# Kernel optimization log

Measured on AMD Instinct MI355X. Metric: run time of the kernel, lower is better.

## Reference

```python
import jax, jax.numpy as jnp
import numpy as np

B, S, N, F = 32, 50, 2000, 3
D = 64
E = 1_000_000
NUM_NODES = B * N


def setup_inputs() -> dict:
    key = jax.random.key(0)
    ks = jax.random.split(key, 8)
    x = jax.random.normal(ks[0], (B, S, N, F), dtype=jnp.float32)
    edge_index = jax.random.randint(ks[1], (2, E), 0, NUM_NODES, dtype=jnp.int64)
    # Glorot-ish init for parameters
    W1 = jax.random.normal(ks[2], (F, D), dtype=jnp.float32) * (1.0 / np.sqrt(F))
    b1 = jnp.zeros((D,), dtype=jnp.float32)
    W2 = jax.random.normal(ks[3], (D, D), dtype=jnp.float32) * (1.0 / np.sqrt(D))
    b2 = jnp.zeros((D,), dtype=jnp.float32)
    Wh = jax.random.normal(ks[4], (D, 2), dtype=jnp.float32) * (1.0 / np.sqrt(D))
    bh = jnp.zeros((2,), dtype=jnp.float32)
    return {"x": x, "edge_index": edge_index, "W1": W1, "b1": b1,
            "W2": W2, "b2": b2, "Wh": Wh, "bh": bh}


def reference(x, edge_index, W1, b1, W2, b2, Wh, bh):
    b, s, n, f = x.shape
    num_nodes = b * n
    h0 = x.mean(axis=1).reshape(num_nodes, f)  # temporal mean, flatten batch graphs

    # GCN normalization with self-loops (PyG GCNConv defaults)
    loops = jnp.arange(num_nodes, dtype=edge_index.dtype)
    src = jnp.concatenate([edge_index[0], loops])
    dst = jnp.concatenate([edge_index[1], loops])
    deg = jax.ops.segment_sum(jnp.ones_like(src, dtype=h0.dtype), dst,
                              num_segments=num_nodes)
    dinv = jnp.where(deg > 0, jax.lax.rsqrt(deg), 0.0)
    norm = dinv[src] * dinv[dst]  # per-edge weight

    def gcn(h, W, bias):
        h = h @ W                                  # transform first (out <= in)
        msg = h[src] * norm[:, None]               # gather + scale
        agg = jax.ops.segment_sum(msg, dst, num_segments=num_nodes)  # scatter-add
        return agg + bias

    h = jax.nn.relu(gcn(h0, W1, b1))
    h = jax.nn.relu(gcn(h, W2, b2))
    # global_mean_pool with batch = arange(B).repeat_interleave(N) == per-graph mean
    pooled = h.reshape(b, n, -1).mean(axis=1)
    return pooled @ Wh + bh
```

## Files before the change

### kernel.cpp

```cpp
#include <hip/hip_runtime.h>
#include <hip/hip_bf16.h>
#include <hip/hip_fp16.h>
#include <cstdint>

#define NV 64000
#define DD 64
#define FF 3
#define NE 1000000
#define BB 32
#define SS 50
#define NN 2000
#define KB 1000
#define CAP 1536
#define NBLKA 250
#define EPB (NE / NBLKA)
#define TMB 750
#define INVALID 0xFFFFFFFFu
#define RPW 16
#define NWAVES (NV / RPW)
#define WPG (NN / RPW)
#define RST 20

__global__ __launch_bounds__(256) void setup_kernel(const int* __restrict__ ei,
                                                    int* __restrict__ flag,
                                                    int* __restrict__ gcur) {
    int i = blockIdx.x * 256 + threadIdx.x;
    if (i < KB) gcur[i] = 0;
    if (blockIdx.x == 0) {
        __shared__ int nz;
        if (threadIdx.x == 0) nz = 0;
        __syncthreads();
        int local = 0;
        for (int k = threadIdx.x; k < 4096; k += 256)
            local |= (ei[2 * k + 1] != 0);
        if (local) atomicOr(&nz, 1);
        __syncthreads();
        if (threadIdx.x == 0) *flag = (nz == 0) ? 1 : 0;
    }
}

__global__ __launch_bounds__(256) void part_tmean_kernel(const int* __restrict__ ei32,
                                                         const int* __restrict__ flag,
                                                         int* __restrict__ gcur,
                                                         unsigned* __restrict__ parts,
                                                         const float* __restrict__ x,
                                                         float* __restrict__ p0) {
    __shared__ unsigned recs[EPB];
    __shared__ int cnt[KB];
    __shared__ int cur[KB];
    int t = threadIdx.x;
    if (blockIdx.x >= NBLKA) {
        int tid = (blockIdx.x - NBLKA) * 256 + t;
        int nf = tid % (NN * FF);
        int b  = tid / (NN * FF);
        const float* xp = x + (size_t)b * SS * NN * FF + nf;
        float acc = 0.f;
        #pragma unroll
        for (int s = 0; s < SS; ++s) acc += xp[(size_t)s * NN * FF];
        p0[tid] = acc * (1.0f / SS);
        return;
    }
    const long long* ei64 = (const long long*)ei32;
    const int is64 = *flag;
    int e0 = blockIdx.x * EPB;
    for (int i = t; i < KB; i += 256) cnt[i] = 0;
    __syncthreads();
    for (int i = t; i < EPB; i += 256) {
        int e = e0 + i;
        int s, d;
        if (is64) { s = (int)ei64[e]; d = (int)ei64[NE + e]; }
        else      { s = ei32[e];      d = ei32[NE + e]; }
        bool ok = (unsigned)s < NV && (unsigned)d < NV;
        recs[i] = ok ? (((unsigned)s << 16) | (unsigned)d) : INVALID;
        if (ok) atomicAdd(&cnt[d >> 6], 1);
    }
    __syncthreads();
    for (int b = t; b < KB; b += 256) {
        int c = cnt[b];
        cur[b] = (c > 0) ? atomicAdd(&gcur[b], c) : 0;
    }
    __syncthreads();
    for (int i = t; i < EPB; i += 256) {
        unsigned r = recs[i];
        if (r != INVALID) {
            int d = (int)(r & 0xFFFFu);
            int b = d >> 6;
            int pos = atomicAdd(&cur[b], 1);
            if (pos < CAP)
                parts[(size_t)b * CAP + pos] = ((r >> 16) << 6) | (unsigned)(d & 63);
        }
    }
}

__global__ __launch_bounds__(256) void bsort_kernel(unsigned* __restrict__ parts,
                                                    const int* __restrict__ gcur,
                                                    int* __restrict__ beg,
                                                    int* __restrict__ end,
                                                    float* __restrict__ dinv,
                                                    float* __restrict__ p0) {
    __shared__ unsigned recs[CAP];
    __shared__ int srt[CAP];
    __shared__ int cnt64[64];
    __shared__ int pref[64];
    __shared__ int cur[64];
    int b = blockIdx.x, t = threadIdx.x;
    int cnt = min(gcur[b], CAP);
    unsigned* p = parts + (size_t)b * CAP;
    if (t < 64) cnt64[t] = 0;
    __syncthreads();
    for (int i = t; i < cnt; i += 256) {
        unsigned r = p[i];
        recs[i] = r;
        atomicAdd(&cnt64[r & 63u], 1);
    }
    __syncthreads();
    if (t < 64) pref[t] = cnt64[t];
    __syncthreads();
    #pragma unroll
    for (int off = 1; off < 64; off <<= 1) {
        int v = (t < 64 && t >= off) ? pref[t - off] : 0;
        __syncthreads();
        if (t < 64) pref[t] += v;
        __syncthreads();
    }
    if (t < 64) {
        int ex = pref[t] - cnt64[t];
        cur[t] = ex;
        int node = (b << 6) + t;
        beg[node] = b * CAP + ex;
        end[node] = b * CAP + ex + cnt64[t];
        dinv[node] = rsqrtf((float)(cnt64[t] + 1));
    }
    __syncthreads();
    for (int i = t; i < cnt; i += 256) {
        unsigned r = recs[i];
        int pos = atomicAdd(&cur[r & 63u], 1);
        srt[pos] = (int)(r >> 6);
    }
    __syncthreads();
    for (int i = t; i < cnt; i += 256) p[i] = (unsigned)srt[i];
    for (int i = t; i < 64 * FF; i += 256) {
        float dv = rsqrtf((float)(cnt64[i / FF] + 1));
        p0[(size_t)b * 64 * FF + i] *= dv;
    }
}

__global__ __launch_bounds__(256) void agg3_kernel(const int* __restrict__ beg,
                                                   const int* __restrict__ end,
                                                   const unsigned* __restrict__ srcs,
                                                   const float* __restrict__ p0,
                                                   const float* __restrict__ dinv,
                                                   float4* __restrict__ q04) {
    int node = blockIdx.x * 256 + threadIdx.x;
    if (node >= NV) return;
    int e = beg[node], en = end[node];
    float a0 = p0[node * 3 + 0], a1 = p0[node * 3 + 1], a2 = p0[node * 3 + 2];
    for (; e + 2 <= en; e += 2) {
        int s0 = srcs[e] * 3, s1 = srcs[e + 1] * 3;
        float u0 = p0[s0], u1 = p0[s0 + 1], u2 = p0[s0 + 2];
        float w0 = p0[s1], w1 = p0[s1 + 1], w2 = p0[s1 + 2];
        a0 += u0 + w0; a1 += u1 + w1; a2 += u2 + w2;
    }
    for (; e < en; ++e) {
        int s = srcs[e] * 3;
        a0 += p0[s]; a1 += p0[s + 1]; a2 += p0[s + 2];
    }
    q04[node] = make_float4(a0, a1, a2, dinv[node]);
}

__global__ void trans1_kernel(const float4* __restrict__ q04,
                              const float* __restrict__ W1, const float* __restrict__ b1,
                              __half2* __restrict__ p1h) {
    int tid = blockIdx.x * blockDim.x + threadIdx.x;
    if (tid >= NV * 32) return;
    int node = tid >> 5, j = tid & 31;
    int d0 = 2 * j, d1 = 2 * j + 1;
    float4 q = q04[node];
    float h0 = fmaf(q.w, fmaf(q.x, W1[d0], fmaf(q.y, W1[64 + d0], q.z * W1[128 + d0])), b1[d0]);
    float h1 = fmaf(q.w, fmaf(q.x, W1[d1], fmaf(q.y, W1[64 + d1], q.z * W1[128 + d1])), b1[d1]);
    p1h[tid] = __floats2half2_rn(q.w * fmaxf(h0, 0.f), q.w * fmaxf(h1, 0.f));
}

__global__ __launch_bounds__(256) void agg64_kernel(const int* __restrict__ beg,
                                                    const int* __restrict__ end,
                                                    const unsigned* __restrict__ srcs,
                                                    const __half2* __restrict__ g,
                                                    float* __restrict__ raw) {
    int lane = threadIdx.x & 63;
    int node = (blockIdx.x * blockDim.x + threadIdx.x) >> 6;
    if (node >= NV) return;
    int grp = lane >> 3, sub = lane & 7;
    const uint4* base = (const uint4*)g;
    float a0 = 0.f, a1 = 0.f, a2 = 0.f, a3 = 0.f;
    float a4 = 0.f, a5 = 0.f, a6 = 0.f, a7 = 0.f;
#define UNPACK_ADD(v) do { float2 f_;                                         \
        f_ = __half22float2(*(const __half2*)&(v).x); a0 += f_.x; a1 += f_.y; \
        f_ = __half22float2(*(const __half2*)&(v).y); a2 += f_.x; a3 += f_.y; \
        f_ = __half22float2(*(const __half2*)&(v).z); a4 += f_.x; a5 += f_.y; \
        f_ = __half22float2(*(const __half2*)&(v).w); a6 += f_.x; a7 += f_.y; } while (0)
    if (grp == 0) {
        uint4 v = base[((size_t)node << 3) + sub];
        UNPACK_ADD(v);
    }
    int e = beg[node] + grp, en = end[node];
    for (; e + 8 < en; e += 16) {
        uint4 v0 = base[((size_t)srcs[e] << 3) + sub];
        uint4 v1 = base[((size_t)srcs[e + 8] << 3) + sub];
        UNPACK_ADD(v0);
        UNPACK_ADD(v1);
    }
    if (e < en) {
        uint4 v = base[((size_t)srcs[e] << 3) + sub];
        UNPACK_ADD(v);
    }
#undef UNPACK_ADD
    #pragma unroll
    for (int m = 8; m <= 32; m <<= 1) {
        a0 += __shfl_xor(a0, m); a1 += __shfl_xor(a1, m);
        a2 += __shfl_xor(a2, m); a3 += __shfl_xor(a3, m);
        a4 += __shfl_xor(a4, m); a5 += __shfl_xor(a5, m);
        a6 += __shfl_xor(a6, m); a7 += __shfl_xor(a7, m);
    }
    if (grp == 0) {
        float4* out = (float4*)(raw + ((size_t)node << 6));
        out[sub * 2 + 0] = make_float4(a0, a1, a2, a3);
        out[sub * 2 + 1] = make_float4(a4, a5, a6, a7);
    }
}

__global__ __launch_bounds__(256) void trans2pool_kernel(const float* __restrict__ q1,
                                                         const float* __restrict__ dinv,
                                                         const float* __restrict__ b2,
                                                         const float* __restrict__ W2,
                                                         float* __restrict__ partials) {
    __shared__ float w2s[64 * 64];
    __shared__ float rT[4][64 * RST];
    int t = threadIdx.x;
    int lane = t & 63, wvid = t >> 6;
    for (int i = t; i < 64 * 64; i += 256) w2s[i] = W2[i];

    int wid = blockIdx.x * 4 + wvid;
    int n0 = wid * RPW;
    float v[16];
    #pragma unroll
    for (int i = 0; i < 16; ++i) v[i] = q1[((size_t)(n0 + i) << 6) + lane];
    float* rw = rT[wvid];
    #pragma unroll
    for (int r0 = 0; r0 < 16; r0 += 4)
        *(float4*)&rw[lane * RST + r0] = make_float4(v[r0], v[r0 + 1], v[r0 + 2], v[r0 + 3]);
    __syncthreads();

    int ri0 = (lane >> 4) * 4;
    int c0 = (lane & 15) * 4;
    float acc00 = 0.f, acc01 = 0.f, acc02 = 0.f, acc03 = 0.f;
    float acc10 = 0.f, acc11 = 0.f, acc12 = 0.f, acc13 = 0.f;
    float acc20 = 0.f, acc21 = 0.f, acc22 = 0.f, acc23 = 0.f;
    float acc30 = 0.f, acc31 = 0.f, acc32 = 0.f, acc33 = 0.f;
    #pragma unroll 2
    for (int k = 0; k < 64; ++k) {
        float4 w4 = *(const float4*)&w2s[k * 64 + c0];
        float4 r4 = *(const float4*)&rw[k * RST + ri0];
        acc00 = fmaf(r4.x, w4.x, acc00); acc01 = fmaf(r4.x, w4.y, acc01);
        acc02 = fmaf(r4.x, w4.z, acc02); acc03 = fmaf(r4.x, w4.w, acc03);
        acc10 = fmaf(r4.y, w4.x, acc10); acc11 = fmaf(r4.y, w4.y, acc11);
        acc12 = fmaf(r4.y, w4.z, acc12); acc13 = fmaf(r4.y, w4.w, acc13);
        acc20 = fmaf(r4.z, w4.x, acc20); acc21 = fmaf(r4.z, w4.y, acc21);
        acc22 = fmaf(r4.z, w4.z, acc22); acc23 = fmaf(r4.z, w4.w, acc23);
        acc30 = fmaf(r4.w, w4.x, acc30); acc31 = fmaf(r4.w, w4.y, acc31);
        acc32 = fmaf(r4.w, w4.z, acc32); acc33 = fmaf(r4.w, w4.w, acc33);
    }
    float4 bv = *(const float4*)&b2[c0];
    float d0 = dinv[n0 + ri0 + 0], d1 = dinv[n0 + ri0 + 1];
    float d2 = dinv[n0 + ri0 + 2], d3 = dinv[n0 + ri0 + 3];
    float s0 = fmaxf(fmaf(d0, acc00, bv.x), 0.f) + fmaxf(fmaf(d1, acc10, bv.x), 0.f)
             + fmaxf(fmaf(d2, acc20, bv.x), 0.f) + fmaxf(fmaf(d3, acc30, bv.x), 0.f);
    float s1 = fmaxf(fmaf(d0, acc01, bv.y), 0.f) + fmaxf(fmaf(d1, acc11, bv.y), 0.f)
             + fmaxf(fmaf(d2, acc21, bv.y), 0.f) + fmaxf(fmaf(d3, acc31, bv.y), 0.f);
    float s2 = fmaxf(fmaf(d0, acc02, bv.z), 0.f) + fmaxf(fmaf(d1, acc12, bv.z), 0.f)
             + fmaxf(fmaf(d2, acc22, bv.z), 0.f) + fmaxf(fmaf(d3, acc32, bv.z), 0.f);
    float s3 = fmaxf(fmaf(d0, acc03, bv.w), 0.f) + fmaxf(fmaf(d1, acc13, bv.w), 0.f)
             + fmaxf(fmaf(d2, acc23, bv.w), 0.f) + fmaxf(fmaf(d3, acc33, bv.w), 0.f);
    s0 += __shfl_xor(s0, 16); s1 += __shfl_xor(s1, 16);
    s2 += __shfl_xor(s2, 16); s3 += __shfl_xor(s3, 16);
    s0 += __shfl_xor(s0, 32); s1 += __shfl_xor(s1, 32);
    s2 += __shfl_xor(s2, 32); s3 += __shfl_xor(s3, 32);
    if (lane < 16)
        *(float4*)&partials[(size_t)wid * 64 + c0] = make_float4(s0, s1, s2, s3);
}

__global__ __launch_bounds__(256) void pool_finish_kernel(const float* __restrict__ partials,
                                                          const float* __restrict__ Wh,
                                                          const float* __restrict__ bh,
                                                          float* __restrict__ out) {
    __shared__ float part[4][64];
    __shared__ float pooled[64];
    int b = blockIdx.x;
    int t = threadIdx.x;
    int d = t & 63, g = t >> 6;
    float s = 0.f;
    for (int c = g; c < WPG; c += 4)
        s += partials[((size_t)(b * WPG + c)) * 64 + d];
    part[g][d] = s;
    __syncthreads();
    if (t < 64)
        pooled[t] = (part[0][t] + part[1][t] + part[2][t] + part[3][t]) * (1.0f / NN);
    __syncthreads();
    if (t < 2) {
        float o = bh[t];
        #pragma unroll 16
        for (int k = 0; k < 64; ++k) o += pooled[k] * Wh[k * 2 + t];
        out[b * 2 + t] = o;
    }
}

extern "C" void kernel_launch(void* const* d_in, const int* in_sizes, int n_in,
                              void* d_out, int out_size, void* d_ws, size_t ws_size,
                              hipStream_t stream) {
    const float* x  = (const float*)d_in[0];
    const int*   ei = (const int*)d_in[1];
    const float* W1 = (const float*)d_in[2];
    const float* b1 = (const float*)d_in[3];
    const float* W2 = (const float*)d_in[4];
    const float* b2 = (const float*)d_in[5];
    const float* Wh = (const float*)d_in[6];
    const float* bh = (const float*)d_in[7];
    float* out = (float*)d_out;

    float* ws   = (float*)d_ws;
    float* bufA = ws;
    float* bufB = bufA + (size_t)NV * DD;
    float* p0   = bufB + (size_t)NV * DD;
    float4* q04 = (float4*)(p0 + (size_t)NV * FF);
    float* dinv = (float*)(q04 + NV);
    float* partials = dinv + NV;
    unsigned* parts = (unsigned*)(partials + (size_t)NWAVES * 64);
    int*   beg  = (int*)(parts + (size_t)KB * CAP);
    int*   end  = beg + NV;
    int*   gcur = end + NV;
    int*   flag = gcur + KB;
    __half2* p1h = (__half2*)bufA;

    setup_kernel<<<4, 256, 0, stream>>>(ei, flag, gcur);
    part_tmean_kernel<<<NBLKA + TMB, 256, 0, stream>>>(ei, flag, gcur, parts, x, p0);

    bsort_kernel<<<KB, 256, 0, stream>>>(parts, gcur, beg, end, dinv, p0);

    agg3_kernel<<<(NV + 255) / 256, 256, 0, stream>>>(beg, end, parts, p0, dinv, q04);

    trans1_kernel<<<NV * 32 / 256, 256, 0, stream>>>(q04, W1, b1, p1h);

    agg64_kernel<<<NV * 64 / 256, 256, 0, stream>>>(beg, end, parts, p1h, bufB);

    trans2pool_kernel<<<NWAVES / 4, 256, 0, stream>>>(bufB, dinv, b2, W2, partials);

    pool_finish_kernel<<<BB, 256, 0, stream>>>(partials, Wh, bh, out);
}
```

Before: 105.4 us.

## Fuse dtype detection into partition kernel, merge agg3 with trans1, store agg64 in half

Removes the setup kernel by having each partition block detect the int64 edge format itself and clearing the bucket counters with a memset. The 3-wide aggregation is fused with the first linear transform through a shared-memory staging of per-node float4s, which eliminates the q04 round trip and one launch. The 64-wide aggregation output is now written as fp16 instead of fp32, halving its write and the following read in trans2pool. In exchange, every partition block redundantly scans 4096 index words, and the layer-2 pre-activations lose some precision.

Measured after the change: 101.1 us, median of 2. -4.1%, faster.

```diff
diff --git a/kernel.cpp b/kernel.cpp
--- a/kernel.cpp
+++ b/kernel.cpp
@@ -21,33 +21,11 @@
 #define WPG (NN / RPW)
 #define RST 20
 
-__global__ __launch_bounds__(256) void setup_kernel(const int* __restrict__ ei,
-                                                    int* __restrict__ flag,
-                                                    int* __restrict__ gcur) {
-    int i = blockIdx.x * 256 + threadIdx.x;
-    if (i < KB) gcur[i] = 0;
-    if (blockIdx.x == 0) {
-        __shared__ int nz;
-        if (threadIdx.x == 0) nz = 0;
-        __syncthreads();
-        int local = 0;
-        for (int k = threadIdx.x; k < 4096; k += 256)
-            local |= (ei[2 * k + 1] != 0);
-        if (local) atomicOr(&nz, 1);
-        __syncthreads();
-        if (threadIdx.x == 0) *flag = (nz == 0) ? 1 : 0;
-    }
-}
-
 __global__ __launch_bounds__(256) void part_tmean_kernel(const int* __restrict__ ei32,
-                                                         const int* __restrict__ flag,
                                                          int* __restrict__ gcur,
                                                          unsigned* __restrict__ parts,
                                                          const float* __restrict__ x,
                                                          float* __restrict__ p0) {
-    __shared__ unsigned recs[EPB];
-    __shared__ int cnt[KB];
-    __shared__ int cur[KB];
     int t = threadIdx.x;
     if (blockIdx.x >= NBLKA) {
         int tid = (blockIdx.x - NBLKA) * 256 + t;
@@ -60,11 +38,20 @@
         p0[tid] = acc * (1.0f / SS);
         return;
     }
+    __shared__ unsigned recs[EPB];
+    __shared__ int cnt[KB];
+    __shared__ int cur[KB];
+    __shared__ int nz;
+    if (t == 0) nz = 0;
+    for (int i = t; i < KB; i += 256) cnt[i] = 0;
+    __syncthreads();
+    int local = 0;
+    for (int k = t; k < 4096; k += 256) local |= (ei32[2 * k + 1] != 0);
+    if (local) atomicOr(&nz, 1);
+    __syncthreads();
+    const int is64 = (nz == 0);
     const long long* ei64 = (const long long*)ei32;
-    const int is64 = *flag;
     int e0 = blockIdx.x * EPB;
-    for (int i = t; i < KB; i += 256) cnt[i] = 0;
-    __syncthreads();
     for (int i = t; i < EPB; i += 256) {
         int e = e0 + i;
         int s, d;
@@ -145,14 +132,17 @@
     }
 }
 
-__global__ __launch_bounds__(256) void agg3_kernel(const int* __restrict__ beg,
-                                                   const int* __restrict__ end,
-                                                   const unsigned* __restrict__ srcs,
-                                                   const float* __restrict__ p0,
-                                                   const float* __restrict__ dinv,
-                                                   float4* __restrict__ q04) {
-    int node = blockIdx.x * 256 + threadIdx.x;
-    if (node >= NV) return;
+__global__ __launch_bounds__(256) void agg3trans_kernel(const int* __restrict__ beg,
+                                                        const int* __restrict__ end,
+                                                        const unsigned* __restrict__ srcs,
+                                                        const float* __restrict__ p0,
+                                                        const float* __restrict__ dinv,
+                                                        const float* __restrict__ W1,
+                                                        const float* __restrict__ b1,
+                                                        __half2* __restrict__ p1h) {
+    __shared__ float4 q4s[256];
+    int t = threadIdx.x;
+    int node = blockIdx.x * 256 + t;
     int e = beg[node], en = end[node];
     float a0 = p0[node * 3 + 0], a1 = p0[node * 3 + 1], a2 = p0[node * 3 + 2];
     for (; e + 2 <= en; e += 2) {
@@ -165,27 +155,28 @@
         int s = srcs[e] * 3;
         a0 += p0[s]; a1 += p0[s + 1]; a2 += p0[s + 2];
     }
-    q04[node] = make_float4(a0, a1, a2, dinv[node]);
-}
-
-__global__ void trans1_kernel(const float4* __restrict__ q04,
-                              const float* __restrict__ W1, const float* __restrict__ b1,
-                              __half2* __restrict__ p1h) {
-    int tid = blockIdx.x * blockDim.x + threadIdx.x;
-    if (tid >= NV * 32) return;
-    int node = tid >> 5, j = tid & 31;
-    int d0 = 2 * j, d1 = 2 * j + 1;
-    float4 q = q04[node];
-    float h0 = fmaf(q.w, fmaf(q.x, W1[d0], fmaf(q.y, W1[64 + d0], q.z * W1[128 + d0])), b1[d0]);
-    float h1 = fmaf(q.w, fmaf(q.x, W1[d1], fmaf(q.y, W1[64 + d1], q.z * W1[128 + d1])), b1[d1]);
-    p1h[tid] = __floats2half2_rn(q.w * fmaxf(h0, 0.f), q.w * fmaxf(h1, 0.f));
+    q4s[t] = make_float4(a0, a1, a2, dinv[node]);
+    __syncthreads();
+    int j = t & 31;
+    int d0 = 2 * j, d1 = d0 + 1;
+    float w00 = W1[d0], w10 = W1[64 + d0], w20 = W1[128 + d0], bb0 = b1[d0];
+    float w01 = W1[d1], w11 = W1[64 + d1], w21 = W1[128 + d1], bb1 = b1[d1];
+    size_t base = (size_t)blockIdx.x * 256 * 32;
+    #pragma unroll 8
+    for (int i = 0; i < 32; ++i) {
+        int idx = t + 256 * i;
+        float4 q = q4s[idx >> 5];
+        float h0 = fmaf(q.w, fmaf(q.x, w00, fmaf(q.y, w10, q.z * w20)), bb0);
+        float h1 = fmaf(q.w, fmaf(q.x, w01, fmaf(q.y, w11, q.z * w21)), bb1);
+        p1h[base + idx] = __floats2half2_rn(q.w * fmaxf(h0, 0.f), q.w * fmaxf(h1, 0.f));
+    }
 }
 
 __global__ __launch_bounds__(256) void agg64_kernel(const int* __restrict__ beg,
                                                     const int* __restrict__ end,
                                                     const unsigned* __restrict__ srcs,
                                                     const __half2* __restrict__ g,
-                                                    float* __restrict__ raw) {
+                                                    __half2* __restrict__ q1h) {
     int lane = threadIdx.x & 63;
     int node = (blockIdx.x * blockDim.x + threadIdx.x) >> 6;
     if (node >= NV) return;
@@ -222,13 +213,16 @@
         a6 += __shfl_xor(a6, m); a7 += __shfl_xor(a7, m);
     }
     if (grp == 0) {
-        float4* out = (float4*)(raw + ((size_t)node << 6));
-        out[sub * 2 + 0] = make_float4(a0, a1, a2, a3);
-        out[sub * 2 + 1] = make_float4(a4, a5, a6, a7);
-    }
-}
-
-__global__ __launch_bounds__(256) void trans2pool_kernel(const float* __restrict__ q1,
+        uint4 o;
+        *(__half2*)&o.x = __floats2half2_rn(a0, a1);
+        *(__half2*)&o.y = __floats2half2_rn(a2, a3);
+        *(__half2*)&o.z = __floats2half2_rn(a4, a5);
+        *(__half2*)&o.w = __floats2half2_rn(a6, a7);
+        ((uint4*)q1h)[((size_t)node << 3) + sub] = o;
+    }
+}
+
+__global__ __launch_bounds__(256) void trans2pool_kernel(const __half* __restrict__ q1h,
                                                          const float* __restrict__ dinv,
                                                          const float* __restrict__ b2,
                                                          const float* __restrict__ W2,
@@ -243,7 +237,8 @@
     int n0 = wid * RPW;
     float v[16];
     #pragma unroll
-    for (int i = 0; i < 16; ++i) v[i] = q1[((size_t)(n0 + i) << 6) + lane];
+    for (int i = 0; i < 16; ++i)
+        v[i] = __half2float(q1h[((size_t)(n0 + i) << 6) + lane]);
     float* rw = rT[wvid];
     #pragma unroll
     for (int r0 = 0; r0 < 16; r0 += 4)
@@ -330,28 +325,25 @@
     float* bufA = ws;
     float* bufB = bufA + (size_t)NV * DD;
     float* p0   = bufB + (size_t)NV * DD;
-    float4* q04 = (float4*)(p0 + (size_t)NV * FF);
-    float* dinv = (float*)(q04 + NV);
+    float* dinv = p0 + (size_t)NV * FF;
     float* partials = dinv + NV;
     unsigned* parts = (unsigned*)(partials + (size_t)NWAVES * 64);
     int*   beg  = (int*)(parts + (size_t)KB * CAP);
     int*   end  = beg + NV;
     int*   gcur = end + NV;
-    int*   flag = gcur + KB;
     __half2* p1h = (__half2*)bufA;
-
-    setup_kernel<<<4, 256, 0, stream>>>(ei, flag, gcur);
-    part_tmean_kernel<<<NBLKA + TMB, 256, 0, stream>>>(ei, flag, gcur, parts, x, p0);
+    __half2* q1h = (__half2*)bufB;
+
+    hipMemsetAsync(gcur, 0, KB * sizeof(int), stream);
+    part_tmean_kernel<<<NBLKA + TMB, 256, 0, stream>>>(ei, gcur, parts, x, p0);
 
     bsort_kernel<<<KB, 256, 0, stream>>>(parts, gcur, beg, end, dinv, p0);
 
-    agg3_kernel<<<(NV + 255) / 256, 256, 0, stream>>>(beg, end, parts, p0, dinv, q04);
-
-    trans1_kernel<<<NV * 32 / 256, 256, 0, stream>>>(q04, W1, b1, p1h);
-
-    agg64_kernel<<<NV * 64 / 256, 256, 0, stream>>>(beg, end, parts, p1h, bufB);
-
-    trans2pool_kernel<<<NWAVES / 4, 256, 0, stream>>>(bufB, dinv, b2, W2, partials);
+    agg3trans_kernel<<<NV / 256, 256, 0, stream>>>(beg, end, parts, p0, dinv, W1, b1, p1h);
+
+    agg64_kernel<<<NV * 64 / 256, 256, 0, stream>>>(beg, end, parts, p1h, q1h);
+
+    trans2pool_kernel<<<NWAVES / 4, 256, 0, stream>>>((const __half*)q1h, dinv, b2, W2, partials);
 
     pool_finish_kernel<<<BB, 256, 0, stream>>>(partials, Wh, bh, out);
 }
```
